# Kernel optimization log

Measured on AMD Instinct MI355X. Metric: run time of the kernel, lower is better.

The kernel has to match this reference:

```python
import jax, jax.numpy as jnp
import numpy as np


def setup_inputs() -> dict:
    key = jax.random.key(0)
    ks = jax.random.split(key, 6)
    B, T = 512, 32768  # batch of audio segments, samples per segment
    return {
        "x": jax.random.normal(ks[0], (B, T), dtype=jnp.float32),
        "g": jax.random.normal(ks[1], (1,), dtype=jnp.float32),
        "r": jax.random.normal(ks[2], (1,), dtype=jnp.float32),
        "m_hp": jax.random.normal(ks[3], (1,), dtype=jnp.float32),
        "m_bp": jax.random.normal(ks[4], (1,), dtype=jnp.float32),
        "m_lp": jax.random.normal(ks[5], (1,), dtype=jnp.float32),
    }


def _biquad_coeffs(g, r, m_hp, m_bp, m_lp):
    # DSVF parameterization: g = tan(pi*sigmoid(g_raw)/2), r = softplus(r_raw)
    gg = jnp.tan(jnp.pi * jax.nn.sigmoid(g) / 2.0)
    rr = jax.nn.softplus(r)
    g2 = gg * gg
    b0 = g2 * m_lp + gg * m_bp + m_hp
    b1 = 2.0 * g2 * m_lp - 2.0 * m_hp
    b2 = g2 * m_lp - gg * m_bp + m_hp
    a0 = g2 + 2.0 * rr * gg + 1.0
    a1 = 2.0 * g2 - 2.0
    a2 = g2 - 2.0 * rr * gg + 1.0
    # scipy.signal.lfilter normalizes by a[0]
    inv_a0 = 1.0 / jnp.squeeze(a0)
    return (jnp.squeeze(b0) * inv_a0, jnp.squeeze(b1) * inv_a0,
            jnp.squeeze(b2) * inv_a0, jnppy_squeeze(a1) * inv_a0 if False else jnp.squeeze(a1) * inv_a0,
            jnp.squeeze(a2) * inv_a0)


def reference(x, g, r, m_hp, m_bp, m_lp):
    """Biquad IIR (direct form II transposed), zero initial state,
    matching scipy.signal.lfilter(b, a, x) along the last axis of x [B, T]."""
    b0, b1, b2, a1, a2 = _biquad_coeffs(g, r, m_hp, m_bp, m_lp)

    def step(carry, xt):  # xt: [B]
        z1, z2 = carry
        y = b0 * xt + z1
        z1n = b1 * xt - a1 * y + z2
        z2n = b2 * xt - a2 * y
        return (z1n, z2n), y

    B = x.shape[0]
    z0 = (jnp.zeros((B,), x.dtype), jnp.zeros((B,), x.dtype))
    _, y_t = jax.lax.scan(step, z0, x.T)  # scan over time: [T, B]
    return y_t.T  # [B, T]
```

## Files before the change

### kernel.cpp

```cpp
#include <hip/hip_runtime.h>
#include <math.h>


namespace {
constexpr int kB = 512;
constexpr int kT = 32768;
constexpr int kChunk = 64;
constexpr int kNChunk = kT / kChunk;
constexpr int kVec = kChunk / 4;
constexpr int kScanThreads = 256;
}

struct CoefBlock {
  double p00, p01, p10, p11;
  float b0, b1, b2, na1, na2;
  float pad[3];
};

__global__ void k_coef(const float* g, const float* r, const float* mhp,
                       const float* mbp, const float* mlp,
                       CoefBlock* __restrict__ cb) {
  double graw = (double)g[0], rraw = (double)r[0];
  double m_hp = (double)mhp[0], m_bp = (double)mbp[0], m_lp = (double)mlp[0];
  double sig = 1.0 / (1.0 + exp(-graw));
  double gg = tan(1.5707963267948966 * sig);
  double rr = (rraw > 30.0) ? rraw : log1p(exp(rraw));
  double g2 = gg * gg;
  double B0 = g2 * m_lp + gg * m_bp + m_hp;
  double B1 = 2.0 * g2 * m_lp - 2.0 * m_hp;
  double B2 = g2 * m_lp - gg * m_bp + m_hp;
  double A0 = g2 + 2.0 * rr * gg + 1.0;
  double A1 = 2.0 * g2 - 2.0;
  double A2 = g2 - 2.0 * rr * gg + 1.0;
  double inv = 1.0 / A0;
  double b0 = B0 * inv, b1 = B1 * inv, b2 = B2 * inv;
  double a1 = A1 * inv, a2 = A2 * inv;
  double m00 = -a1, m01 = 1.0, m10 = -a2, m11 = 0.0;
  for (int i = 0; i < 6; ++i) {
    double t00 = m00 * m00 + m01 * m10;
    double t01 = m00 * m01 + m01 * m11;
    double t10 = m10 * m00 + m11 * m10;
    double t11 = m10 * m01 + m11 * m11;
    m00 = t00; m01 = t01; m10 = t10; m11 = t11;
  }
  cb->p00 = m00; cb->p01 = m01; cb->p10 = m10; cb->p11 = m11;
  cb->b0 = (float)b0; cb->b1 = (float)b1; cb->b2 = (float)b2;
  cb->na1 = (float)(-a1); cb->na2 = (float)(-a2);
}

#define IIR_STEP(xx, yy)                                         \
  do {                                                           \
    yy = fmaf(b0, xx, z1);                                       \
    z1 = fmaf(na1, yy, fmaf(b1, xx, z2));                        \
    z2 = fmaf(na2, yy, b2 * xx);                                 \
  } while (0)

__global__ __launch_bounds__(256) void k_partial(
    const float* __restrict__ x, const CoefBlock* __restrict__ cb,
    float2* __restrict__ st) {
  int tid = blockIdx.x * 256 + threadIdx.x;
  int row = tid >> 9;
  int chunk = tid & (kNChunk - 1);

  float b0 = cb->b0, b1 = cb->b1, b2 = cb->b2, na1 = cb->na1, na2 = cb->na2;

  const float4* xv =
      (const float4*)(x + (size_t)row * kT + (size_t)chunk * kChunk);
  float4 v[kVec];
#pragma unroll
  for (int i = 0; i < kVec; ++i) v[i] = xv[i];

  float z1 = 0.f, z2 = 0.f;
#pragma unroll
  for (int i = 0; i < kVec; ++i) {
    float y;
    IIR_STEP(v[i].x, y); IIR_STEP(v[i].y, y);
    IIR_STEP(v[i].z, y); IIR_STEP(v[i].w, y);
  }
  st[(size_t)row * kNChunk + chunk] = make_float2(z1, z2);
}

__global__ __launch_bounds__(kScanThreads) void k_scan(
    float2* __restrict__ st, const CoefBlock* __restrict__ cb) {
  int row = blockIdx.x;
  int t = threadIdx.x;
  double p00 = cb->p00, p01 = cb->p01, p10 = cb->p10, p11 = cb->p11;

  float2* rowp = st + (size_t)row * kNChunk;
  float4 ld = ((const float4*)rowp)[t];
  double d0x = (double)ld.x, d0y = (double)ld.y;
  double d1x = (double)ld.z, d1y = (double)ld.w;

  double a1v = p00 * d0x + p01 * d0y + d1x;
  double a2v = p10 * d0x + p11 * d0y + d1y;
  double w00 = p00 * p00 + p01 * p10, w01 = p00 * p01 + p01 * p11;
  double w10 = p10 * p00 + p11 * p10, w11 = p10 * p01 + p11 * p11;

  __shared__ double s1[kScanThreads], s2[kScanThreads];
  for (int o = 1; o < kScanThreads; o <<= 1) {
    s1[t] = a1v; s2[t] = a2v;
    __syncthreads();
    double q1 = 0.0, q2 = 0.0;
    if (t >= o) { q1 = s1[t - o]; q2 = s2[t - o]; }
    __syncthreads();
    a1v += w00 * q1 + w01 * q2;
    a2v += w10 * q1 + w11 * q2;
    double t00 = w00 * w00 + w01 * w10, t01 = w00 * w01 + w01 * w11;
    double t10 = w10 * w00 + w11 * w10, t11 = w10 * w01 + w11 * w11;
    w00 = t00; w01 = t01; w10 = t10; w11 = t11;
  }
  s1[t] = a1v; s2[t] = a2v;
  __syncthreads();
  double e1 = 0.0, e2 = 0.0;
  if (t > 0) { e1 = s1[t - 1]; e2 = s2[t - 1]; }
  double i1 = p00 * e1 + p01 * e2 + d0x;
  double i2 = p10 * e1 + p11 * e2 + d0y;
  ((float4*)rowp)[t] = make_float4((float)e1, (float)e2, (float)i1, (float)i2);
}

__global__ __launch_bounds__(256) void k_final(
    const float* __restrict__ x, const float2* __restrict__ st,
    const CoefBlock* __restrict__ cb, float* __restrict__ out) {
  int tid = blockIdx.x * 256 + threadIdx.x;
  int row = tid >> 9;
  int chunk = tid & (kNChunk - 1);

  float b0 = cb->b0, b1 = cb->b1, b2 = cb->b2, na1 = cb->na1, na2 = cb->na2;

  float2 s0 = st[(size_t)row * kNChunk + chunk];
  float z1 = s0.x, z2 = s0.y;

  const float4* xv =
      (const float4*)(x + (size_t)row * kT + (size_t)chunk * kChunk);
  float4* yv = (float4*)(out + (size_t)row * kT + (size_t)chunk * kChunk);
  float4 v[kVec];
#pragma unroll
  for (int i = 0; i < kVec; ++i) v[i] = xv[i];

#pragma unroll
  for (int i = 0; i < kVec; ++i) {
    float4 o;
    IIR_STEP(v[i].x, o.x); IIR_STEP(v[i].y, o.y);
    IIR_STEP(v[i].z, o.z); IIR_STEP(v[i].w, o.w);
    yv[i] = o;
  }
}

extern "C" void kernel_launch(void* const* d_in, const int* in_sizes, int n_in,
                              void* d_out, int out_size, void* d_ws,
                              size_t ws_size, hipStream_t stream) {
  const float* x   = (const float*)d_in[0];
  const float* g   = (const float*)d_in[1];
  const float* r   = (const float*)d_in[2];
  const float* mhp = (const float*)d_in[3];
  const float* mbp = (const float*)d_in[4];
  const float* mlp = (const float*)d_in[5];
  float* out = (float*)d_out;

  CoefBlock* cb = (CoefBlock*)d_ws;
  float2* st = (float2*)((char*)d_ws + 256);

  const int nthreads = kB * kNChunk;
  k_coef<<<1, 1, 0, stream>>>(g, r, mhp, mbp, mlp, cb);
  k_partial<<<nthreads / 256, 256, 0, stream>>>(x, cb, st);
  k_scan<<<kB, kScanThreads, 0, stream>>>(st, cb);
  k_final<<<nthreads / 256, 256, 0, stream>>>(x, st, cb, out);
}
```

Before: 157.6 us.

## Coalesce chunk loads/stores via padded LDS transpose and fold coefficient kernel into consumers

Each 64-thread block now loads its 64 contiguous chunks with lane-strided float4 reads. It transposes them through padded shared memory so every thread still scans its own chunk, and k_final uses the same LDS transpose on the way out so output stores are coalesced. This replaces the old per-thread loads and stores of 256 contiguous bytes, which were uncoalesced across a wavefront. The separate single-thread coefficient kernel is removed and every kernel recomputes the coefficients in float32 instead, which drops one launch but changes precision relative to the old double-precision computation. Costs added are LDS traffic, a barrier, and smaller 64-thread blocks.

```diff
diff --git a/kernel.cpp b/kernel.cpp
--- a/kernel.cpp
+++ b/kernel.cpp
@@ -7,35 +7,87 @@
 constexpr int kT = 32768;
 constexpr int kChunk = 64;
 constexpr int kNChunk = kT / kChunk;
-constexpr int kVec = kChunk / 4;
 constexpr int kScanThreads = 256;
-}
-
-struct CoefBlock {
-  double p00, p01, p10, p11;
-  float b0, b1, b2, na1, na2;
-  float pad[3];
-};
-
-__global__ void k_coef(const float* g, const float* r, const float* mhp,
-                       const float* mbp, const float* mlp,
-                       CoefBlock* __restrict__ cb) {
-  double graw = (double)g[0], rraw = (double)r[0];
-  double m_hp = (double)mhp[0], m_bp = (double)mbp[0], m_lp = (double)mlp[0];
-  double sig = 1.0 / (1.0 + exp(-graw));
-  double gg = tan(1.5707963267948966 * sig);
-  double rr = (rraw > 30.0) ? rraw : log1p(exp(rraw));
-  double g2 = gg * gg;
-  double B0 = g2 * m_lp + gg * m_bp + m_hp;
-  double B1 = 2.0 * g2 * m_lp - 2.0 * m_hp;
-  double B2 = g2 * m_lp - gg * m_bp + m_hp;
-  double A0 = g2 + 2.0 * rr * gg + 1.0;
-  double A1 = 2.0 * g2 - 2.0;
-  double A2 = g2 - 2.0 * rr * gg + 1.0;
-  double inv = 1.0 / A0;
-  double b0 = B0 * inv, b1 = B1 * inv, b2 = B2 * inv;
-  double a1 = A1 * inv, a2 = A2 * inv;
-  double m00 = -a1, m01 = 1.0, m10 = -a2, m11 = 0.0;
+constexpr int kStride = kChunk + 1;
+}
+
+__device__ inline void coeffs_f32(const float* g, const float* r,
+                                  const float* mhp, const float* mbp,
+                                  const float* mlp, float& b0, float& b1,
+                                  float& b2, float& a1, float& a2) {
+  float graw = g[0], rraw = r[0];
+  float sig = 1.0f / (1.0f + expf(-graw));
+  float gg = tanf(1.5707963267948966f * sig);
+  float rr = (rraw > 20.0f) ? rraw : log1pf(expf(rraw));
+  float g2 = gg * gg;
+  float m_hp = mhp[0], m_bp = mbp[0], m_lp = mlp[0];
+  float B0 = g2 * m_lp + gg * m_bp + m_hp;
+  float B1 = 2.0f * g2 * m_lp - 2.0f * m_hp;
+  float B2 = g2 * m_lp - gg * m_bp + m_hp;
+  float A0 = g2 + 2.0f * rr * gg + 1.0f;
+  float A1 = 2.0f * g2 - 2.0f;
+  float A2 = g2 - 2.0f * rr * gg + 1.0f;
+  float inv = 1.0f / A0;
+  b0 = B0 * inv; b1 = B1 * inv; b2 = B2 * inv;
+  a1 = A1 * inv; a2 = A2 * inv;
+}
+
+#define IIR_STEP(xx, yy)                                         \
+  do {                                                           \
+    yy = fmaf(b0, xx, z1);                                       \
+    z1 = fmaf(na1, yy, fmaf(b1, xx, z2));                        \
+    z2 = fmaf(na2, yy, b2 * xx);                                 \
+  } while (0)
+
+__global__ __launch_bounds__(64) void k_partial(
+    const float* __restrict__ x, const float* g, const float* r,
+    const float* mhp, const float* mbp, const float* mlp,
+    float2* __restrict__ st) {
+  __shared__ float buf[64 * kStride];
+  int lane = threadIdx.x;
+
+  float b0, b1, b2, a1, a2;
+  coeffs_f32(g, r, mhp, mbp, mlp, b0, b1, b2, a1, a2);
+  float na1 = -a1, na2 = -a2;
+
+  const float4* xv = (const float4*)x + (size_t)blockIdx.x * 1024;
+  float4 v[16];
+#pragma unroll
+  for (int i = 0; i < 16; ++i) v[i] = xv[i * 64 + lane];
+
+#pragma unroll
+  for (int i = 0; i < 16; ++i) {
+    int f = i * 64 + lane;
+    int base = (f >> 4) * kStride + ((f & 15) << 2);
+    buf[base] = v[i].x; buf[base + 1] = v[i].y;
+    buf[base + 2] = v[i].z; buf[base + 3] = v[i].w;
+  }
+  __syncthreads();
+#pragma unroll
+  for (int i = 0; i < 16; ++i) {
+    int base = lane * kStride + (i << 2);
+    v[i] = make_float4(buf[base], buf[base + 1], buf[base + 2], buf[base + 3]);
+  }
+
+  float z1 = 0.f, z2 = 0.f;
+#pragma unroll
+  for (int i = 0; i < 16; ++i) {
+    float y;
+    IIR_STEP(v[i].x, y); IIR_STEP(v[i].y, y);
+    IIR_STEP(v[i].z, y); IIR_STEP(v[i].w, y);
+  }
+  st[(size_t)blockIdx.x * 64 + lane] = make_float2(z1, z2);
+}
+
+__global__ __launch_bounds__(kScanThreads) void k_scan(
+    float2* __restrict__ st, const float* g, const float* r,
+    const float* mhp, const float* mbp, const float* mlp) {
+  int row = blockIdx.x;
+  int t = threadIdx.x;
+
+  float b0f, b1f, b2f, a1f, a2f;
+  coeffs_f32(g, r, mhp, mbp, mlp, b0f, b1f, b2f, a1f, a2f);
+  double m00 = -(double)a1f, m01 = 1.0, m10 = -(double)a2f, m11 = 0.0;
   for (int i = 0; i < 6; ++i) {
     double t00 = m00 * m00 + m01 * m10;
     double t01 = m00 * m01 + m01 * m11;
@@ -43,48 +95,7 @@
     double t11 = m10 * m01 + m11 * m11;
     m00 = t00; m01 = t01; m10 = t10; m11 = t11;
   }
-  cb->p00 = m00; cb->p01 = m01; cb->p10 = m10; cb->p11 = m11;
-  cb->b0 = (float)b0; cb->b1 = (float)b1; cb->b2 = (float)b2;
-  cb->na1 = (float)(-a1); cb->na2 = (float)(-a2);
-}
-
-#define IIR_STEP(xx, yy)                                         \
-  do {                                                           \
-    yy = fmaf(b0, xx, z1);                                       \
-    z1 = fmaf(na1, yy, fmaf(b1, xx, z2));                        \
-    z2 = fmaf(na2, yy, b2 * xx);                                 \
-  } while (0)
-
-__global__ __launch_bounds__(256) void k_partial(
-    const float* __restrict__ x, const CoefBlock* __restrict__ cb,
-    float2* __restrict__ st) {
-  int tid = blockIdx.x * 256 + threadIdx.x;
-  int row = tid >> 9;
-  int chunk = tid & (kNChunk - 1);
-
-  float b0 = cb->b0, b1 = cb->b1, b2 = cb->b2, na1 = cb->na1, na2 = cb->na2;
-
-  const float4* xv =
-      (const float4*)(x + (size_t)row * kT + (size_t)chunk * kChunk);
-  float4 v[kVec];
-#pragma unroll
-  for (int i = 0; i < kVec; ++i) v[i] = xv[i];
-
-  float z1 = 0.f, z2 = 0.f;
-#pragma unroll
-  for (int i = 0; i < kVec; ++i) {
-    float y;
-    IIR_STEP(v[i].x, y); IIR_STEP(v[i].y, y);
-    IIR_STEP(v[i].z, y); IIR_STEP(v[i].w, y);
-  }
-  st[(size_t)row * kNChunk + chunk] = make_float2(z1, z2);
-}
-
-__global__ __launch_bounds__(kScanThreads) void k_scan(
-    float2* __restrict__ st, const CoefBlock* __restrict__ cb) {
-  int row = blockIdx.x;
-  int t = threadIdx.x;
-  double p00 = cb->p00, p01 = cb->p01, p10 = cb->p10, p11 = cb->p11;
+  double p00 = m00, p01 = m01, p10 = m10, p11 = m11;
 
   float2* rowp = st + (size_t)row * kNChunk;
   float4 ld = ((const float4*)rowp)[t];
@@ -118,31 +129,59 @@
   ((float4*)rowp)[t] = make_float4((float)e1, (float)e2, (float)i1, (float)i2);
 }
 
-__global__ __launch_bounds__(256) void k_final(
+__global__ __launch_bounds__(64) void k_final(
     const float* __restrict__ x, const float2* __restrict__ st,
-    const CoefBlock* __restrict__ cb, float* __restrict__ out) {
-  int tid = blockIdx.x * 256 + threadIdx.x;
-  int row = tid >> 9;
-  int chunk = tid & (kNChunk - 1);
-
-  float b0 = cb->b0, b1 = cb->b1, b2 = cb->b2, na1 = cb->na1, na2 = cb->na2;
-
-  float2 s0 = st[(size_t)row * kNChunk + chunk];
+    const float* g, const float* r, const float* mhp, const float* mbp,
+    const float* mlp, float* __restrict__ out) {
+  __shared__ float buf[64 * kStride];
+  int lane = threadIdx.x;
+
+  float b0, b1, b2, a1, a2;
+  coeffs_f32(g, r, mhp, mbp, mlp, b0, b1, b2, a1, a2);
+  float na1 = -a1, na2 = -a2;
+
+  const float4* xv = (const float4*)x + (size_t)blockIdx.x * 1024;
+  float4 v[16];
+#pragma unroll
+  for (int i = 0; i < 16; ++i) v[i] = xv[i * 64 + lane];
+
+#pragma unroll
+  for (int i = 0; i < 16; ++i) {
+    int f = i * 64 + lane;
+    int base = (f >> 4) * kStride + ((f & 15) << 2);
+    buf[base] = v[i].x; buf[base + 1] = v[i].y;
+    buf[base + 2] = v[i].z; buf[base + 3] = v[i].w;
+  }
+  __syncthreads();
+#pragma unroll
+  for (int i = 0; i < 16; ++i) {
+    int base = lane * kStride + (i << 2);
+    v[i] = make_float4(buf[base], buf[base + 1], buf[base + 2], buf[base + 3]);
+  }
+
+  float2 s0 = st[(size_t)blockIdx.x * 64 + lane];
   float z1 = s0.x, z2 = s0.y;
-
-  const float4* xv =
-      (const float4*)(x + (size_t)row * kT + (size_t)chunk * kChunk);
-  float4* yv = (float4*)(out + (size_t)row * kT + (size_t)chunk * kChunk);
-  float4 v[kVec];
-#pragma unroll
-  for (int i = 0; i < kVec; ++i) v[i] = xv[i];
-
-#pragma unroll
-  for (int i = 0; i < kVec; ++i) {
+#pragma unroll
+  for (int i = 0; i < 16; ++i) {
     float4 o;
     IIR_STEP(v[i].x, o.x); IIR_STEP(v[i].y, o.y);
     IIR_STEP(v[i].z, o.z); IIR_STEP(v[i].w, o.w);
-    yv[i] = o;
+    v[i] = o;
+  }
+
+#pragma unroll
+  for (int i = 0; i < 16; ++i) {
+    int base = lane * kStride + (i << 2);
+    buf[base] = v[i].x; buf[base + 1] = v[i].y;
+    buf[base + 2] = v[i].z; buf[base + 3] = v[i].w;
+  }
+  __syncthreads();
+  float4* yv = (float4*)out + (size_t)blockIdx.x * 1024;
+#pragma unroll
+  for (int i = 0; i < 16; ++i) {
+    int f = i * 64 + lane;
+    int base = (f >> 4) * kStride + ((f & 15) << 2);
+    yv[f] = make_float4(buf[base], buf[base + 1], buf[base + 2], buf[base + 3]);
   }
 }
 
@@ -156,13 +195,10 @@
   const float* mbp = (const float*)d_in[4];
   const float* mlp = (const float*)d_in[5];
   float* out = (float*)d_out;
-
-  CoefBlock* cb = (CoefBlock*)d_ws;
-  float2* st = (float2*)((char*)d_ws + 256);
-
-  const int nthreads = kB * kNChunk;
-  k_coef<<<1, 1, 0, stream>>>(g, r, mhp, mbp, mlp, cb);
-  k_partial<<<nthreads / 256, 256, 0, stream>>>(x, cb, st);
-  k_scan<<<kB, kScanThreads, 0, stream>>>(st, cb);
-  k_final<<<nthreads / 256, 256, 0, stream>>>(x, st, cb, out);
-}
+  float2* st = (float2*)d_ws;
+
+  const int nblocks = kB * kNChunk / 64;
+  k_partial<<<nblocks, 64, 0, stream>>>(x, g, r, mhp, mbp, mlp, st);
+  k_scan<<<kB, kScanThreads, 0, stream>>>(st, g, r, mhp, mbp, mlp);
+  k_final<<<nblocks, 64, 0, stream>>>(x, st, g, r, mhp, mbp, mlp, out);
+}
```

Result: faster. 135.5 us (-14.0%).
